# Performance work log

Measured on AMD Instinct MI355X. Metric: run time of the kernel, lower is better.

Reference implementation:

```python
import jax, jax.numpy as jnp
import numpy as np

D_MODEL = 2048
N_HEADS = 32
N_KV_HEADS = 8
D_K = D_MODEL // N_HEADS
HEADS_PER_GROUP = N_HEADS // N_KV_HEADS
B, S = 2, 2048


def setup_inputs() -> dict:
    key = jax.random.key(0)
    ks = jax.random.split(key, 12)
    scale = 1.0 / np.sqrt(D_MODEL)
    inp = {
        "q": jax.random.normal(ks[0], (B, S, D_MODEL), jnp.float32),
        "k": jax.random.normal(ks[1], (B, S, D_MODEL), jnp.float32),
        "v": jax.random.normal(ks[2], (B, S, D_MODEL), jnp.float32),
        # causal mask, broadcastable over [B, H, S, S]
        "mask": jnp.tril(jnp.ones((S, S), jnp.bool_))[None, None],
        # torch Linear convention: W [out, in], y = x @ W.T + b
        "Wq": jax.random.normal(ks[3], (D_MODEL, D_MODEL), jnp.float32) * scale,
        "bq": jax.random.normal(ks[4], (D_MODEL,), jnp.float32) * 0.01,
        "Wk": jax.random.normal(ks[5], (N_KV_HEADS * D_K, D_MODEL), jnp.float32) * scale,
        "bk": jax.random.normal(ks[6], (N_KV_HEADS * D_K,), jnp.float32) * 0.01,
        "Wv": jax.random.normal(ks[7], (N_KV_HEADS * D_K, D_MODEL), jnp.float32) * scale,
        "bv": jax.random.normal(ks[8], (N_KV_HEADS * D_K,), jnp.float32) * 0.01,
        "Wo": jax.random.normal(ks[9], (D_MODEL, D_MODEL), jnp.float32) * scale,
        "bo": jax.random.normal(ks[10], (D_MODEL,), jnp.float32) * 0.01,
    }
    return inp


def reference(q, k, v, mask, Wq, bq, Wk, bk, Wv, bv, Wo, bo):
    b, s, _ = q.shape
    # projections (torch Linear: x @ W.T + b)
    query = q @ Wq.T + bq                      # [B, S, D]
    key = k @ Wk.T + bk                        # [B, S, Kv*dk]
    value = v @ Wv.T + bv
    # [B, Kv, G, S, dk] for query (group heads per kv head instead of repeating K/V)
    query = query.reshape(b, s, N_KV_HEADS, HEADS_PER_GROUP, D_K).transpose(0, 2, 3, 1, 4)
    key = key.reshape(b, s, N_KV_HEADS, D_K).transpose(0, 2, 1, 3)      # [B, Kv, S, dk]
    value = value.reshape(b, s, N_KV_HEADS, D_K).transpose(0, 2, 1, 3)  # [B, Kv, S, dk]
    scores = jnp.einsum('bkgqd,bksd->bkgqs', query, key) / jnp.sqrt(jnp.float32(D_K))
    # mask is [1,1,S,S] broadcastable; add group axis
    scores = jnp.where(mask[:, :, None], scores, jnp.float32(-1e9))
    attn = jax.nn.softmax(scores, axis=-1)     # dropout p=0.0 -> identity
    out = jnp.einsum('bkgqs,bksd->bkgqd', attn, value)  # [B, Kv, G, S, dk]
    out = out.transpose(0, 3, 1, 2, 4).reshape(b, s, D_MODEL)
    return out @ Wo.T + bo
```

## Files before the change

### kernel.cpp

```cpp
#include <hip/hip_runtime.h>
#include <cstdint>

#define D_MODEL 2048
#define NKV 8
#define GQ 4
#define DK 64
#define B_ 2
#define S_ 2048
#define MS (B_*S_)
#define KVD (NKV*DK)

typedef unsigned short u16;
typedef __attribute__((ext_vector_type(8))) short bf16x8;
typedef __attribute__((ext_vector_type(4))) short bf16x4;
typedef __attribute__((ext_vector_type(4))) float f32x4;
typedef __attribute__((ext_vector_type(16))) float f32x16;
typedef __attribute__((ext_vector_type(4))) unsigned short u16x4;

__device__ __forceinline__ u16 f2bf(float f) {
    union { float f; uint32_t u; } x; x.f = f;
    uint32_t u = x.u;
    uint32_t r = (u + 0x7FFFu + ((u >> 16) & 1u)) >> 16;
    return (u16)r;
}
__device__ __forceinline__ float bf2f(u16 h) {
    union { uint32_t u; float f; } x; x.u = ((uint32_t)h) << 16;
    return x.f;
}

__device__ __forceinline__ void gload_lds16(const void* g, void* lds) {
    __builtin_amdgcn_global_load_lds(
        (const __attribute__((address_space(1))) void*)g,
        (__attribute__((address_space(3))) void*)lds, 16, 0, 0);
}

__device__ __forceinline__ bf16x8 cvt8(float4 a, float4 b) {
    union { unsigned u[4]; bf16x8 v; } r;
    asm("v_cvt_pk_bf16_f32 %0, %1, %2" : "=v"(r.u[0]) : "v"(a.x), "v"(a.y));
    asm("v_cvt_pk_bf16_f32 %0, %1, %2" : "=v"(r.u[1]) : "v"(a.z), "v"(a.w));
    asm("v_cvt_pk_bf16_f32 %0, %1, %2" : "=v"(r.u[2]) : "v"(b.x), "v"(b.y));
    asm("v_cvt_pk_bf16_f32 %0, %1, %2" : "=v"(r.u[3]) : "v"(b.z), "v"(b.w));
    return r.v;
}

__device__ __forceinline__ bf16x8 frag_f32(const char* S, int R, int fq) {
    int s0 = ((2 * fq) ^ (R & 7)) * 16;
    int s1 = ((2 * fq + 1) ^ (R & 7)) * 16;
    float4 a = *(const float4*)(S + R * 128 + s0);
    float4 b = *(const float4*)(S + R * 128 + s1);
    return cvt8(a, b);
}

__global__ __launch_bounds__(256, 3)
void gemm_qkv(const float* __restrict__ Aq, const float* __restrict__ Ak,
              const float* __restrict__ Av,
              const float* __restrict__ Wq, const float* __restrict__ Wk,
              const float* __restrict__ Wv,
              const float* __restrict__ bq, const float* __restrict__ bk,
              const float* __restrict__ bv,
              u16* __restrict__ Qp, u16* __restrict__ Kp, u16* __restrict__ Vt) {
    __shared__ __align__(16) char SA[128 * 128];
    __shared__ __align__(16) char SB[128 * 128];
    const int tid = threadIdx.x;
    const int lane = tid & 63;
    const int fr = lane & 15, fq = lane >> 4;
    const int w = tid >> 6;
    const int wr = w >> 1, wc = w & 1;
    const int K = D_MODEL, NT = K / 32;

    const int bid = blockIdx.x;
    const int sw = (bid & 7) * 96 + (bid >> 3);
    const float* A; const float* Bw; const float* bias;
    int seg, by, bx;
    if (sw < 512)      { seg = 0; A = Aq; Bw = Wq; bias = bq; by = sw >> 4;         bx = sw & 15; }
    else if (sw < 640) { seg = 1; A = Ak; Bw = Wk; bias = bk; by = (sw - 512) >> 2; bx = (sw - 512) & 3; }
    else               { seg = 2; A = Av; Bw = Wv; bias = bv; by = (sw - 640) >> 2; bx = (sw - 640) & 3; }
    const int m0 = by * 128, n0 = bx * 128;

    f32x4 acc[4][4] = {};
    const int arow = wr * 64, brow = wc * 64;
    const int wb16 = (tid & 192) * 16;

    for (int t = 0; t < NT; ++t) {
        const int k0 = t << 5;
#pragma unroll
        for (int j = 0; j < 4; ++j) {
            int idx = j * 256 + tid;
            int r = idx >> 3, p = idx & 7;
            int c = (p ^ (r & 7)) * 4;
            gload_lds16(A  + (size_t)(m0 + r) * K + k0 + c, SA + j * 4096 + wb16);
            gload_lds16(Bw + (size_t)(n0 + r) * K + k0 + c, SB + j * 4096 + wb16);
        }
        __syncthreads();
        bf16x8 af[4], bfr[4];
#pragma unroll
        for (int m = 0; m < 4; ++m) af[m] = frag_f32(SA, arow + m * 16 + fr, fq);
#pragma unroll
        for (int n = 0; n < 4; ++n) bfr[n] = frag_f32(SB, brow + n * 16 + fr, fq);
        __builtin_amdgcn_s_setprio(1);
#pragma unroll
        for (int m = 0; m < 4; ++m)
#pragma unroll
            for (int n = 0; n < 4; ++n)
                acc[m][n] = __builtin_amdgcn_mfma_f32_16x16x32_bf16(af[m], bfr[n], acc[m][n], 0, 0, 0);
        __builtin_amdgcn_s_setprio(0);
        __syncthreads();
    }

    float bvv[4];
#pragma unroll
    for (int n = 0; n < 4; ++n) bvv[n] = bias[n0 + brow + n * 16 + fr];
#pragma unroll
    for (int m = 0; m < 4; ++m) {
        int grow0 = m0 + arow + m * 16 + fq * 4;
#pragma unroll
        for (int n = 0; n < 4; ++n) {
            int gcol = n0 + brow + n * 16 + fr;
#pragma unroll
            for (int r = 0; r < 4; ++r) {
                float v = acc[m][n][r] + bvv[n];
                int grow = grow0 + r;
                if (seg == 0)      Qp[(size_t)grow * D_MODEL + gcol] = f2bf(v);
                else if (seg == 1) Kp[(size_t)grow * KVD + gcol] = f2bf(v);
                else {
                    int b = grow >> 11, s = grow & (S_ - 1);
                    Vt[((size_t)b * KVD + gcol) * S_ + s] = f2bf(v);
                }
            }
        }
    }
}

__global__ __launch_bounds__(256, 2)
void gemm_o(const u16* __restrict__ A, const float* __restrict__ Bw,
            const float* __restrict__ bias, float* __restrict__ Cout) {
    __shared__ __align__(16) char SAo[2][128 * 64];
    __shared__ __align__(16) char SBo[2][128 * 128];
    const int tid = threadIdx.x;
    const int lane = tid & 63;
    const int fr = lane & 15, fq = lane >> 4;
    const int w = tid >> 6;
    const int wr = w >> 1, wc = w & 1;
    const int K = D_MODEL, N = D_MODEL, NT = K / 32;

    const int bid = blockIdx.x;
    const int sw = (bid & 7) * 64 + (bid >> 3);
    const int by = sw >> 4, bx = sw & 15;
    const int m0 = by * 128, n0 = bx * 128;
    const int wb16 = (tid & 192) * 16;

    auto STAGE = [&](int t, int qb) {
        const int k0 = t << 5;
#pragma unroll
        for (int j = 0; j < 2; ++j) {
            int idx = j * 256 + tid;
            int r = idx >> 2, p = idx & 3;
            gload_lds16(A + (size_t)(m0 + r) * K + k0 + p * 8, SAo[qb] + j * 4096 + wb16);
        }
#pragma unroll
        for (int j = 0; j < 4; ++j) {
            int idx = j * 256 + tid;
            int r = idx >> 3, p = idx & 7;
            int c = (p ^ (r & 7)) * 4;
            gload_lds16(Bw + (size_t)(n0 + r) * K + k0 + c, SBo[qb] + j * 4096 + wb16);
        }
    };

    f32x4 acc[4][4] = {};
    const int arow = wr * 64, brow = wc * 64;

    STAGE(0, 0);
    STAGE(1, 1);
    asm volatile("s_waitcnt vmcnt(6)" ::: "memory");
    __builtin_amdgcn_s_barrier();

    for (int t = 0; t < NT; ++t) {
        const int qb = t & 1;
        const char* sa = SAo[qb];
        const char* sb = SBo[qb];
        bf16x8 af[4], bfr[4];
#pragma unroll
        for (int m = 0; m < 4; ++m) {
            int R = arow + m * 16 + fr;
            af[m] = *(const bf16x8*)(sa + R * 64 + fq * 16);
        }
#pragma unroll
        for (int n = 0; n < 4; ++n) bfr[n] = frag_f32(sb, brow + n * 16 + fr, fq);
        __builtin_amdgcn_s_setprio(1);
#pragma unroll
        for (int m = 0; m < 4; ++m)
#pragma unroll
            for (int n = 0; n < 4; ++n)
                acc[m][n] = __builtin_amdgcn_mfma_f32_16x16x32_bf16(af[m], bfr[n], acc[m][n], 0, 0, 0);
        __builtin_amdgcn_s_setprio(0);
        if (t + 1 < NT) {
            __builtin_amdgcn_s_barrier();
            if (t + 2 < NT) {
                STAGE(t + 2, qb);
                asm volatile("s_waitcnt vmcnt(6)" ::: "memory");
            } else {
                asm volatile("s_waitcnt vmcnt(0)" ::: "memory");
            }
            __builtin_amdgcn_s_barrier();
        }
    }

    float bvv[4];
#pragma unroll
    for (int n = 0; n < 4; ++n) bvv[n] = bias[n0 + brow + n * 16 + fr];
#pragma unroll
    for (int m = 0; m < 4; ++m) {
        int grow0 = m0 + arow + m * 16 + fq * 4;
#pragma unroll
        for (int n = 0; n < 4; ++n) {
            int gcol = n0 + brow + n * 16 + fr;
#pragma unroll
            for (int r = 0; r < 4; ++r)
                Cout[(size_t)(grow0 + r) * N + gcol] = acc[m][n][r] + bvv[n];
        }
    }
}

__global__ __launch_bounds__(256, 4)
void attn_fwd(const u16* __restrict__ Qp, const u16* __restrict__ Kp,
              const u16* __restrict__ Vt, u16* __restrict__ AO) {
    __shared__ __align__(16) u16 Klds[2][4096];
    __shared__ __align__(16) u16 Vlds[2][4096];
    const int bid = blockIdx.x;
    const int qblk = 15 - (bid >> 6);
    const int rest = bid & 63;
    const int b = rest >> 5;
    const int kv = (rest >> 2) & 7;
    const int g = rest & 3;
    const int tid = threadIdx.x, w = tid >> 6, l = tid & 63;
    const int q31 = l & 31, hi = l >> 5;
    const int h = kv * GQ + g;
    const int qw = qblk * 128 + w * 32;
    const int q0 = qw + q31;

    const u16* kbase = Kp + (size_t)(b * S_) * KVD + kv * DK;
    const u16* vbase = Vt + ((size_t)b * KVD + kv * DK) * S_;

    const float SCALE = 0.125f * 1.44269504f;
    bf16x8 qf[4];
    const u16* qp = Qp + ((size_t)(b * S_) + q0) * D_MODEL + h * DK;
#pragma unroll
    for (int ks = 0; ks < 4; ++ks) {
        bf16x8 t = *(const bf16x8*)(qp + ks * 16 + hi * 8);
#pragma unroll
        for (int j = 0; j < 8; ++j) t[j] = (short)f2bf(bf2f((u16)t[j]) * SCALE);
        qf[ks] = t;
    }

    const int nt = 2 * qblk + 2;
    const int bound = (qw + 31) >> 6;

    auto STAGE = [&](int t, int bufsel) {
#pragma unroll
        for (int r = 0; r < 2; ++r) {
            int idx = r * 256 + tid;
            int row = idx >> 3;
            int slotK = (idx & 7) ^ (row & 7);
            int jV = (idx & 7) ^ ((row >> 1) & 7);
            u16* kdst = &Klds[bufsel][(r * 256 + w * 64) * 8];
            u16* vdst = &Vlds[bufsel][(r * 256 + w * 64) * 8];
            gload_lds16(kbase + (size_t)(t * 64 + row) * KVD + slotK * 8, kdst);
            gload_lds16(vbase + (size_t)row * S_ + t * 64 + jV * 8, vdst);
        }
    };

    f32x16 o0 = {}, o1 = {};
    float m_run = -1e30f, l_run = 0.f;

    STAGE(0, 0);
    __syncthreads();
    int cur = 0;
    for (int t = 0; t < nt; ++t) {
        if (t + 1 < nt) STAGE(t + 1, cur ^ 1);
        if (t <= bound) {
            const u16* Kc = Klds[cur];
            const u16* Vc = Vlds[cur];
            const int base0 = t * 64, base1 = t * 64 + 32;
            const bool act1 = (base1 <= qw + 31);

            f32x16 s0 = {};
            {
                const int row = q31;
#pragma unroll
                for (int ks = 0; ks < 4; ++ks) {
                    bf16x8 kf = *(const bf16x8*)&Kc[row * 64 + ((((ks << 1) | hi)) ^ (row & 7)) * 8];
                    s0 = __builtin_amdgcn_mfma_f32_32x32x16_bf16(kf, qf[ks], s0, 0, 0, 0);
                }
            }
            f32x16 s1 = {};
            if (act1) {
                const int row = 32 + q31;
#pragma unroll
                for (int ks = 0; ks < 4; ++ks) {
                    bf16x8 kf = *(const bf16x8*)&Kc[row * 64 + ((((ks << 1) | hi)) ^ (row & 7)) * 8];
                    s1 = __builtin_amdgcn_mfma_f32_32x32x16_bf16(kf, qf[ks], s1, 0, 0, 0);
                }
            }
            if (base0 + 31 > qw) {
#pragma unroll
                for (int r = 0; r < 16; ++r) {
                    int koff = (r & 3) + 8 * (r >> 2) + 4 * hi;
                    s0[r] = (base0 + koff <= q0) ? s0[r] : -1e30f;
                }
            }
            if (act1 && (base1 + 31 > qw)) {
#pragma unroll
                for (int r = 0; r < 16; ++r) {
                    int koff = (r & 3) + 8 * (r >> 2) + 4 * hi;
                    s1[r] = (base1 + koff <= q0) ? s1[r] : -1e30f;
                }
            }
            float pm = s0[0];
#pragma unroll
            for (int r = 1; r < 16; ++r) pm = fmaxf(pm, s0[r]);
            if (act1) {
#pragma unroll
                for (int r = 0; r < 16; ++r) pm = fmaxf(pm, s1[r]);
            }
            pm = fmaxf(pm, __shfl_xor(pm, 32));
            if (__any(pm > m_run + 8.0f)) {
                float mn = fmaxf(m_run, pm);
                float sc = __builtin_amdgcn_exp2f(m_run - mn);
                m_run = mn; l_run *= sc;
#pragma unroll
                for (int r = 0; r < 16; ++r) { o0[r] *= sc; o1[r] *= sc; }
            }
            float psum = 0.f;
#pragma unroll
            for (int r = 0; r < 16; ++r) { float p = __builtin_amdgcn_exp2f(s0[r] - m_run); s0[r] = p; psum += p; }
            if (act1) {
#pragma unroll
                for (int r = 0; r < 16; ++r) { float p = __builtin_amdgcn_exp2f(s1[r] - m_run); s1[r] = p; psum += p; }
            }
            l_run += psum;
            unsigned W0[8], W1[8];
#pragma unroll
            for (int tt = 0; tt < 8; ++tt)
                asm("v_cvt_pk_bf16_f32 %0, %1, %2" : "=v"(W0[tt]) : "v"(s0[2 * tt]), "v"(s0[2 * tt + 1]));
            if (act1) {
#pragma unroll
                for (int tt = 0; tt < 8; ++tt)
                    asm("v_cvt_pk_bf16_f32 %0, %1, %2" : "=v"(W1[tt]) : "v"(s1[2 * tt]), "v"(s1[2 * tt + 1]));
            }
#pragma unroll
            for (int sl = 0; sl < 2; ++sl) {
                union { unsigned u[4]; bf16x8 v; } bw;
#pragma unroll
                for (int i = 0; i < 4; ++i) bw.u[i] = W0[sl * 4 + i];
#pragma unroll
                for (int half = 0; half < 2; ++half) {
                    const int row = half * 32 + q31;
                    union { bf16x4 h4[2]; bf16x8 v; } vf;
                    int sa = (sl * 4 + hi) ^ (row & 14);
                    int sb = (sl * 4 + 2 + hi) ^ (row & 14);
                    vf.h4[0] = *(const bf16x4*)&Vc[row * 64 + sa * 4];
                    vf.h4[1] = *(const bf16x4*)&Vc[row * 64 + sb * 4];
                    if (half == 0) o0 = __builtin_amdgcn_mfma_f32_32x32x16_bf16(vf.v, bw.v, o0, 0, 0, 0);
                    else           o1 = __builtin_amdgcn_mfma_f32_32x32x16_bf16(vf.v, bw.v, o1, 0, 0, 0);
                }
            }
            if (act1) {
#pragma unroll
                for (int sl = 2; sl < 4; ++sl) {
                    union { unsigned u[4]; bf16x8 v; } bw;
#pragma unroll
                    for (int i = 0; i < 4; ++i) bw.u[i] = W1[(sl - 2) * 4 + i];
#pragma unroll
                    for (int half = 0; half < 2; ++half) {
                        const int row = half * 32 + q31;
                        union { bf16x4 h4[2]; bf16x8 v; } vf;
                        int sa = (sl * 4 + hi) ^ (row & 14);
                        int sb = (sl * 4 + 2 + hi) ^ (row & 14);
                        vf.h4[0] = *(const bf16x4*)&Vc[row * 64 + sa * 4];
                        vf.h4[1] = *(const bf16x4*)&Vc[row * 64 + sb * 4];
                        if (half == 0) o0 = __builtin_amdgcn_mfma_f32_32x32x16_bf16(vf.v, bw.v, o0, 0, 0, 0);
                        else           o1 = __builtin_amdgcn_mfma_f32_32x32x16_bf16(vf.v, bw.v, o1, 0, 0, 0);
                    }
                }
            }
        }
        __syncthreads();
        cur ^= 1;
    }

    float lt = l_run + __shfl_xor(l_run, 32);
    float rl = 1.0f / lt;
    u16* op = AO + ((size_t)(b * S_) + q0) * D_MODEL + h * DK;
#pragma unroll
    for (int half = 0; half < 2; ++half) {
#pragma unroll
        for (int rr = 0; rr < 16; rr += 4) {
            u16x4 pk;
#pragma unroll
            for (int i = 0; i < 4; ++i)
                pk[i] = f2bf((half ? o1[rr + i] : o0[rr + i]) * rl);
            *(u16x4*)(op + half * 32 + (rr >> 2) * 8 + 4 * hi) = pk;
        }
    }
}

extern "C" void kernel_launch(void* const* d_in, const int* in_sizes, int n_in,
                              void* d_out, int out_size, void* d_ws, size_t ws_size,
                              hipStream_t stream) {
    const float* q  = (const float*)d_in[0];
    const float* k  = (const float*)d_in[1];
    const float* v  = (const float*)d_in[2];
    const float* Wq = (const float*)d_in[4];
    const float* bq = (const float*)d_in[5];
    const float* Wk = (const float*)d_in[6];
    const float* bk = (const float*)d_in[7];
    const float* Wv = (const float*)d_in[8];
    const float* bv = (const float*)d_in[9];
    const float* Wo = (const float*)d_in[10];
    const float* bo = (const float*)d_in[11];
    float* out = (float*)d_out;

    char* ws = (char*)d_ws;
    size_t off = 0;
    auto alloc = [&](size_t bytes) -> void* {
        void* p = ws + off;
        off += (bytes + 255) & ~(size_t)255;
        return p;
    };
    u16* Qp = (u16*)alloc((size_t)MS * D_MODEL * 2);
    u16* Kp = (u16*)alloc((size_t)MS * KVD * 2);
    u16* Vt = (u16*)alloc((size_t)MS * KVD * 2);
    u16* AO = (u16*)alloc((size_t)MS * D_MODEL * 2);

    gemm_qkv<<<768, 256, 0, stream>>>(q, k, v, Wq, Wk, Wv, bq, bk, bv, Qp, Kp, Vt);

    attn_fwd<<<16 * 64, 256, 0, stream>>>(Qp, Kp, Vt, AO);

    gemm_o<<<512, 256, 0, stream>>>(AO, Wo, bo, out);
}
```

Baseline: 219.1 us.

## Re-swizzle GEMM LDS tiles into k-halves and raise attention MFMA priority

```diff
diff --git a/kernel.cpp b/kernel.cpp
--- a/kernel.cpp
+++ b/kernel.cpp
@@ -44,10 +44,11 @@
 }
 
 __device__ __forceinline__ bf16x8 frag_f32(const char* S, int R, int fq) {
-    int s0 = ((2 * fq) ^ (R & 7)) * 16;
-    int s1 = ((2 * fq + 1) ^ (R & 7)) * 16;
-    float4 a = *(const float4*)(S + R * 128 + s0);
-    float4 b = *(const float4*)(S + R * 128 + s1);
+    const char* base = S + (fq >> 1) * 8192 + R * 64;
+    const int rho = (R >> 1) & 3;
+    const int g0 = (2 * fq) & 3;
+    float4 a = *(const float4*)(base + ((g0 ^ rho) << 4));
+    float4 b = *(const float4*)(base + (((g0 + 1) ^ rho) << 4));
     return cvt8(a, b);
 }
 
@@ -59,8 +60,8 @@
               const float* __restrict__ bq, const float* __restrict__ bk,
               const float* __restrict__ bv,
               u16* __restrict__ Qp, u16* __restrict__ Kp, u16* __restrict__ Vt) {
-    __shared__ __align__(16) char SA[128 * 128];
-    __shared__ __align__(16) char SB[128 * 128];
+    __shared__ __align__(16) char SA[16384];
+    __shared__ __align__(16) char SB[16384];
     const int tid = threadIdx.x;
     const int lane = tid & 63;
     const int fr = lane & 15, fq = lane >> 4;
@@ -86,10 +87,11 @@
 #pragma unroll
         for (int j = 0; j < 4; ++j) {
             int idx = j * 256 + tid;
-            int r = idx >> 3, p = idx & 7;
-            int c = (p ^ (r & 7)) * 4;
-            gload_lds16(A  + (size_t)(m0 + r) * K + k0 + c, SA + j * 4096 + wb16);
-            gload_lds16(Bw + (size_t)(n0 + r) * K + k0 + c, SB + j * 4096 + wb16);
+            int h = idx >> 9, R = (idx >> 2) & 127, sl = idx & 3;
+            int c = sl ^ ((R >> 1) & 3);
+            int koff = k0 + h * 16 + c * 4;
+            gload_lds16(A  + (size_t)(m0 + R) * K + koff, SA + j * 4096 + wb16);
+            gload_lds16(Bw + (size_t)(n0 + R) * K + koff, SB + j * 4096 + wb16);
         }
         __syncthreads();
         bf16x8 af[4], bfr[4];
@@ -134,8 +136,8 @@
 __global__ __launch_bounds__(256, 2)
 void gemm_o(const u16* __restrict__ A, const float* __restrict__ Bw,
             const float* __restrict__ bias, float* __restrict__ Cout) {
-    __shared__ __align__(16) char SAo[2][128 * 64];
-    __shared__ __align__(16) char SBo[2][128 * 128];
+    __shared__ __align__(16) char SAo[2][8192];
+    __shared__ __align__(16) char SBo[2][16384];
     const int tid = threadIdx.x;
     const int lane = tid & 63;
     const int fr = lane & 15, fq = lane >> 4;
@@ -154,15 +156,16 @@
 #pragma unroll
         for (int j = 0; j < 2; ++j) {
             int idx = j * 256 + tid;
-            int r = idx >> 2, p = idx & 3;
-            gload_lds16(A + (size_t)(m0 + r) * K + k0 + p * 8, SAo[qb] + j * 4096 + wb16);
+            int R = idx >> 2, sl = idx & 3;
+            int c = sl ^ ((R >> 1) & 3);
+            gload_lds16(A + (size_t)(m0 + R) * K + k0 + c * 8, SAo[qb] + j * 4096 + wb16);
         }
 #pragma unroll
         for (int j = 0; j < 4; ++j) {
             int idx = j * 256 + tid;
-            int r = idx >> 3, p = idx & 7;
-            int c = (p ^ (r & 7)) * 4;
-            gload_lds16(Bw + (size_t)(n0 + r) * K + k0 + c, SBo[qb] + j * 4096 + wb16);
+            int h = idx >> 9, R = (idx >> 2) & 127, sl = idx & 3;
+            int c = sl ^ ((R >> 1) & 3);
+            gload_lds16(Bw + (size_t)(n0 + R) * K + k0 + h * 16 + c * 4, SBo[qb] + j * 4096 + wb16);
         }
     };
 
@@ -182,7 +185,7 @@
 #pragma unroll
         for (int m = 0; m < 4; ++m) {
             int R = arow + m * 16 + fr;
-            af[m] = *(const bf16x8*)(sa + R * 64 + fq * 16);
+            af[m] = *(const bf16x8*)(sa + R * 64 + ((fq ^ ((R >> 1) & 3)) << 4));
         }
 #pragma unroll
         for (int n = 0; n < 4; ++n) bfr[n] = frag_f32(sb, brow + n * 16 + fr, fq);
@@ -284,6 +287,7 @@
             const bool act1 = (base1 <= qw + 31);
 
             f32x16 s0 = {};
+            __builtin_amdgcn_s_setprio(1);
             {
                 const int row = q31;
 #pragma unroll
@@ -301,6 +305,7 @@
                     s1 = __builtin_amdgcn_mfma_f32_32x32x16_bf16(kf, qf[ks], s1, 0, 0, 0);
                 }
             }
+            __builtin_amdgcn_s_setprio(0);
             if (base0 + 31 > qw) {
 #pragma unroll
                 for (int r = 0; r < 16; ++r) {
@@ -347,6 +352,7 @@
                 for (int tt = 0; tt < 8; ++tt)
                     asm("v_cvt_pk_bf16_f32 %0, %1, %2" : "=v"(W1[tt]) : "v"(s1[2 * tt]), "v"(s1[2 * tt + 1]));
             }
+            __builtin_amdgcn_s_setprio(1);
 #pragma unroll
             for (int sl = 0; sl < 2; ++sl) {
                 union { unsigned u[4]; bf16x8 v; } bw;
@@ -383,6 +389,7 @@
                     }
                 }
             }
+            __builtin_amdgcn_s_setprio(0);
         }
         __syncthreads();
         cur ^= 1;
```

Measured after the change: 231.5 us. 1.06x slower.
